# Optimization experiments

Hardware: AMD Instinct MI355X
Metric: run time of the kernel (lower is better)

The kernel has to match this reference:

```python
import jax, jax.numpy as jnp
import numpy as np

D_IN = 1024
D_OUT = 1024
H = 16            # head_cnt
G = 4             # attention_groups
LF = 2            # linformer_factor
HEAD_OUT = D_OUT // H          # 64 (value head dim)
DQ = HEAD_OUT // LF            # 32 (query/key head dim)
B, T = 2, 2048


def setup_inputs() -> dict:
    key = jax.random.key(0)
    ks = jax.random.split(key, 7)
    s = 0.02
    return {
        "x": jax.random.normal(ks[0], (B, T, D_IN), dtype=jnp.float32),
        "Wq": jax.random.normal(ks[1], (D_IN, D_OUT // LF), dtype=jnp.float32) * s,
        "Wk": jax.random.normal(ks[2], (D_IN, (D_OUT // LF) // G), dtype=jnp.float32) * s,
        "Wv": jax.random.normal(ks[3], (D_IN, D_OUT // G), dtype=jnp.float32) * s,
        "Wp": jax.random.normal(ks[4], (D_OUT, D_OUT), dtype=jnp.float32) * s,
        "bp": jnp.zeros((D_OUT,), dtype=jnp.float32),
    }


def _alibi_bias(T, dtype):
    # standard ALiBi slopes for H heads (H is a power of 2): m_h = 2^(-8h/H), h=1..H
    slopes = jnp.asarray(2.0 ** (-8.0 * np.arange(1, H + 1) / H), dtype=dtype)
    pos = jnp.arange(T)
    rel = (pos[None, :] - pos[:, None]).astype(dtype)  # j - i, <= 0 on causal part
    return slopes[:, None, None] * rel[None, :, :]      # (H, T, T)


def reference(x, Wq, Wk, Wv, Wp, bp):
    b, t, _ = x.shape
    q = x @ Wq                                  # (b, t, D_OUT/LF)
    k = jnp.tile(x @ Wk, (1, 1, G))             # repeat KV groups -> (b, t, D_OUT/LF)
    v = jnp.tile(x @ Wv, (1, 1, G))             # (b, t, D_OUT)

    q = q.reshape(b, t, H, DQ).transpose(0, 2, 1, 3)        # (b, H, t, DQ)
    k = k.reshape(b, t, H, DQ).transpose(0, 2, 1, 3)
    v = v.reshape(b, t, H, HEAD_OUT).transpose(0, 2, 1, 3)  # (b, H, t, HEAD_OUT)

    scores = jnp.einsum('bhqd,bhkd->bhqk', q, k)            # (b, H, t, t)
    causal = jnp.triu(jnp.ones((t, t), dtype=bool), k=1)
    scores = jnp.where(causal, -jnp.inf, scores)
    # faithful to source: alibi added after masking, then scaled by 1/sqrt(d_k)
    scores = (scores + _alibi_bias(t, scores.dtype)) / jnp.sqrt(jnp.asarray(DQ, scores.dtype))
    w = jax.nn.softmax(scores, axis=-1)
    ctx = jnp.einsum('bhqk,bhkd->bqhd', w, v).reshape(b, t, D_OUT)
    return ctx @ Wp + bp
```

## Files before the change

kernel.cpp:

```cpp
#include <hip/hip_runtime.h>
#include <hip/hip_bf16.h>

#define T_SEQ 2048
#define H_CNT 16
#define B_SZ  2
#define QKV_LD 896
#define KOFF   512
#define VOFF   640

typedef float  f32x4   __attribute__((ext_vector_type(4)));
typedef float  f32x16  __attribute__((ext_vector_type(16)));
typedef __bf16 bf16x8  __attribute__((ext_vector_type(8)));

static __device__ __forceinline__ ushort f2bf(float f) {
    union { float f; unsigned u; } v; v.f = f;
    unsigned u = v.u;
    unsigned r = (u + 0x7fffu + ((u >> 16) & 1u)) >> 16;
    return (ushort)r;
}
static __device__ __forceinline__ unsigned pack2bf(float a, float b) {
    union { __bf16 h[2]; unsigned u; } pk;
    pk.h[0] = (__bf16)a; pk.h[1] = (__bf16)b;
    return pk.u;
}

static __device__ __forceinline__ f32x4 mfma16(bf16x8 a, bf16x8 b, f32x4 c) {
    return __builtin_amdgcn_mfma_f32_16x16x32_bf16(a, b, c, 0, 0, 0);
}
static __device__ __forceinline__ f32x16 mfma32(bf16x8 a, bf16x8 b, f32x16 c) {
    return __builtin_amdgcn_mfma_f32_32x32x16_bf16(a, b, c, 0, 0, 0);
}

static __device__ __forceinline__ void gl_lds16(const void* g, void* l) {
    __builtin_amdgcn_global_load_lds((const __attribute__((address_space(1))) void*)g,
                                     (__attribute__((address_space(3))) void*)l, 16, 0, 0);
}

__global__ __launch_bounds__(256) void convert_bf16(const float* __restrict__ src,
                                                    ushort* __restrict__ dst) {
    const int i = blockIdx.x * 256 + threadIdx.x;
    const float4 v0 = reinterpret_cast<const float4*>(src)[i * 2];
    const float4 v1 = reinterpret_cast<const float4*>(src)[i * 2 + 1];
    uint4 o;
    o.x = (unsigned)f2bf(v0.x) | ((unsigned)f2bf(v0.y) << 16);
    o.y = (unsigned)f2bf(v0.z) | ((unsigned)f2bf(v0.w) << 16);
    o.z = (unsigned)f2bf(v1.x) | ((unsigned)f2bf(v1.y) << 16);
    o.w = (unsigned)f2bf(v1.z) | ((unsigned)f2bf(v1.w) << 16);
    reinterpret_cast<uint4*>(dst)[i] = o;
}

__global__ __launch_bounds__(256) void prep_weights(const float* __restrict__ Wq,
                                                    const float* __restrict__ Wk,
                                                    const float* __restrict__ Wv,
                                                    const float* __restrict__ Wp,
                                                    ushort* __restrict__ Wqkvt,
                                                    ushort* __restrict__ Wpt) {
    __shared__ float tile[32][33];
    const int x = blockIdx.x;
    const float* src; ushort* dst; int C, cx;
    if (x < 16)      { src = Wq; dst = Wqkvt;              C = 512;  cx = x; }
    else if (x < 20) { src = Wk; dst = Wqkvt + 512 * 1024; C = 128;  cx = x - 16; }
    else if (x < 28) { src = Wv; dst = Wqkvt + 640 * 1024; C = 256;  cx = x - 20; }
    else             { src = Wp; dst = Wpt;                C = 1024; cx = x - 28; }
    const int tx = threadIdx.x & 31, ty = threadIdx.x >> 5;
    const int r0 = blockIdx.y * 32, c0 = cx * 32;
#pragma unroll
    for (int i = 0; i < 32; i += 8)
        tile[ty + i][tx] = src[(size_t)(r0 + ty + i) * C + c0 + tx];
    __syncthreads();
#pragma unroll
    for (int i = 0; i < 32; i += 8)
        dst[(size_t)(c0 + ty + i) * 1024 + r0 + tx] = f2bf(tile[tx][ty + i]);
}

__global__ __launch_bounds__(256) void transpose_bf16_str(const ushort* __restrict__ src,
                                                          int src_ld, size_t src_zoff,
                                                          ushort* __restrict__ dst,
                                                          int R, int C, size_t dst_zoff) {
    __shared__ ushort tile[32][33];
    const int tx = threadIdx.x & 31, ty = threadIdx.x >> 5;
    const int r0 = blockIdx.y * 32, c0 = blockIdx.x * 32;
    const ushort* s = src + (size_t)blockIdx.z * src_zoff;
    ushort* d = dst + (size_t)blockIdx.z * dst_zoff;
#pragma unroll
    for (int i = 0; i < 32; i += 8)
        tile[ty + i][tx] = s[(size_t)(r0 + ty + i) * src_ld + c0 + tx];
    __syncthreads();
#pragma unroll
    for (int i = 0; i < 32; i += 8)
        d[(size_t)(c0 + ty + i) * R + r0 + tx] = tile[tx][ty + i];
}

template <bool OUT_BF16>
__global__ __launch_bounds__(256) void gemm_bf16(const ushort* __restrict__ A,
                                                 const ushort* __restrict__ Bt,
                                                 const float* __restrict__ bias,
                                                 void* __restrict__ Cout,
                                                 int M, int N, int K) {
    __shared__ __align__(16) ushort Aa[64 * 32], Ab[64 * 32];
    __shared__ __align__(16) ushort Ba[128 * 32], Bb[128 * 32];

    const int tid = threadIdx.x;
    const int w = tid >> 6, l = tid & 63;
    const int bm = blockIdx.y * 64, bn = blockIdx.x * 128;
    const int wr = (w >> 1) * 32, wc = (w & 1) * 64;
    const int lr = l & 15, lk = (l >> 4) * 8;
    const int crow = l >> 2, ck8 = (l & 3) * 8;

    const ushort* Ag  = A + (size_t)(bm + w * 16 + crow) * K + ck8;
    const ushort* Bg0 = Bt + (size_t)(bn + w * 16 + crow) * K + ck8;
    const ushort* Bg1 = Bt + (size_t)(bn + (w + 4) * 16 + crow) * K + ck8;
    ushort* Ala  = &Aa[w * 16 * 32];
    ushort* Alb  = &Ab[w * 16 * 32];
    ushort* Bl0a = &Ba[w * 16 * 32];
    ushort* Bl0b = &Bb[w * 16 * 32];
    ushort* Bl1a = &Ba[(w + 4) * 16 * 32];
    ushort* Bl1b = &Bb[(w + 4) * 16 * 32];

    f32x4 acc[2][4];
#pragma unroll
    for (int m = 0; m < 2; ++m)
#pragma unroll
        for (int n = 0; n < 4; ++n) acc[m][n] = (f32x4){0.f, 0.f, 0.f, 0.f};

    for (int k0 = 0; k0 < K; k0 += 64) {
        __syncthreads();
        gl_lds16(Ag + k0, Ala);
        gl_lds16(Ag + k0 + 32, Alb);
        gl_lds16(Bg0 + k0, Bl0a);
        gl_lds16(Bg0 + k0 + 32, Bl0b);
        gl_lds16(Bg1 + k0, Bl1a);
        gl_lds16(Bg1 + k0 + 32, Bl1b);
        __syncthreads();

        bf16x8 af0[2], af1[2], bf0[4], bf1[4];
#pragma unroll
        for (int m = 0; m < 2; ++m) {
            af0[m] = *reinterpret_cast<const bf16x8*>(&Aa[(wr + m * 16 + lr) * 32 + lk]);
            af1[m] = *reinterpret_cast<const bf16x8*>(&Ab[(wr + m * 16 + lr) * 32 + lk]);
        }
#pragma unroll
        for (int n = 0; n < 4; ++n) {
            bf0[n] = *reinterpret_cast<const bf16x8*>(&Ba[(wc + n * 16 + lr) * 32 + lk]);
            bf1[n] = *reinterpret_cast<const bf16x8*>(&Bb[(wc + n * 16 + lr) * 32 + lk]);
        }
#pragma unroll
        for (int m = 0; m < 2; ++m)
#pragma unroll
            for (int n = 0; n < 4; ++n) {
                acc[m][n] = mfma16(af0[m], bf0[n], acc[m][n]);
                acc[m][n] = mfma16(af1[m], bf1[n], acc[m][n]);
            }
    }

    const int orow = bm + wr + (l >> 4) * 4;
    const int ocol0 = bn + wc + lr;
#pragma unroll
    for (int m = 0; m < 2; ++m)
#pragma unroll
        for (int n = 0; n < 4; ++n) {
            const int col = ocol0 + n * 16;
            const float bv = OUT_BF16 ? 0.0f : bias[col];
#pragma unroll
            for (int r = 0; r < 4; ++r) {
                const size_t idx = (size_t)(orow + m * 16 + r) * N + col;
                if constexpr (OUT_BF16)
                    reinterpret_cast<ushort*>(Cout)[idx] = f2bf(acc[m][n][r]);
                else
                    reinterpret_cast<float*>(Cout)[idx] = acc[m][n][r] + bv;
            }
        }
}

#define LDK 40
#define LDV 136

__global__ __launch_bounds__(1024) void attn_mfma8(const ushort* __restrict__ qkv,
                                                   const ushort* __restrict__ vT,
                                                   ushort* __restrict__ ctx) {
    __shared__ __align__(16) ushort Ks[2][128 * LDK];
    __shared__ __align__(16) ushort Vs[2][64 * LDV];
    __shared__ float lsred[3][4][32];

    const int tid = threadIdx.x;
    const int w = tid >> 6, l = tid & 63;
    const int lq = l & 31;
    const int hi = l >> 5;
    const int tp = blockIdx.x, g = blockIdx.y, b = blockIdx.z;
    const int hd = w & 3, grp = w >> 2;
    const int h = g + 4 * hd;

    const float slope = exp2f(-0.5f * (float)(h + 1));
    const float k1 = 0.17677669529663687f * 1.4426950408889634f;
    const float k2 = slope * k1;
    const int Wint = (int)(275.0f / slope);

    const int ksd = tid >> 2, kc4 = tid & 3;
    const ushort* kgp = qkv + (size_t)b * T_SEQ * QKV_LD + KOFF + g * 32 +
                        (size_t)ksd * QKV_LD + kc4 * 8;
    const int sv = tid & 511;
    const int vsd = sv >> 3, vj = sv & 7;
    const int vs0 = (vj >> 2) << 1, vc4 = vj & 3;
    const int voff = (vc4 & 1) * 4 + (vc4 >> 1) * 16;
    const ushort* vgp = vT + ((size_t)b * 256 + g * 64 + vsd) * T_SEQ + vs0 * 32 + vc4 * 8;
    const int vl0 = vsd * LDV + vs0 * 32 + voff;
    const int vl1 = vsd * LDV + (vs0 + 1) * 32 + voff;

    float* slotA = reinterpret_cast<float*>(&Ks[0][0]);
    float* slotB = reinterpret_cast<float*>(&Vs[0][0]);
    float* slotC = reinterpret_cast<float*>(&Vs[1][0]);
    const int sidx = (hd * 64 + l) * 16;

    int cur = 0;
    for (int ph = 0; ph < 2; ++ph) {
        const int t = ph ? tp : (63 - tp);
        const int i0 = t * 32;
        const int nkeys = i0 + 32;
        const int jtmax = (nkeys + 127) & ~127;

        const ushort* qrow = qkv + ((size_t)(b * T_SEQ + i0 + lq)) * QKV_LD + h * 32 + hi * 8;
        const bf16x8 qa = *reinterpret_cast<const bf16x8*>(qrow);
        const bf16x8 qb = *reinterpret_cast<const bf16x8*>(qrow + 16);

        f32x16 o0, o1;
#pragma unroll
        for (int r = 0; r < 16; ++r) { o0[r] = 0.0f; o1[r] = 0.0f; }
        float ls = 0.0f;

        uint4 kreg, vr0, vr1;
        if (tid < 512) {
            kreg = *reinterpret_cast<const uint4*>(kgp);
        } else {
            vr0 = *reinterpret_cast<const uint4*>(vgp);
            vr1 = *reinterpret_cast<const uint4*>(vgp + 32);
        }

        for (int jt = 0; jt < jtmax; jt += 128) {
            if (tid < 512) {
                *reinterpret_cast<uint4*>(&Ks[cur][ksd * LDK + kc4 * 8]) = kreg;
            } else {
                *reinterpret_cast<uint2*>(&Vs[cur][vl0]) = make_uint2(vr0.x, vr0.y);
                *reinterpret_cast<uint2*>(&Vs[cur][vl0 + 8]) = make_uint2(vr0.z, vr0.w);
                *reinterpret_cast<uint2*>(&Vs[cur][vl1]) = make_uint2(vr1.x, vr1.y);
                *reinterpret_cast<uint2*>(&Vs[cur][vl1 + 8]) = make_uint2(vr1.z, vr1.w);
            }
            const int jn = jt + 128;
            if (jn < jtmax) {
                if (tid < 512) {
                    kreg = *reinterpret_cast<const uint4*>(kgp + (size_t)jn * QKV_LD);
                } else {
                    vr0 = *reinterpret_cast<const uint4*>(vgp + jn);
                    vr1 = *reinterpret_cast<const uint4*>(vgp + jn + 32);
                }
            }
            __syncthreads();

            const int jts = jt + 32 * grp;
            if (jts < nkeys && jts + 31 >= i0 - Wint) {
                const bf16x8 ka = *reinterpret_cast<const bf16x8*>(&Ks[cur][(grp * 32 + lq) * LDK + hi * 8]);
                const bf16x8 kb2 = *reinterpret_cast<const bf16x8*>(&Ks[cur][(grp * 32 + lq) * LDK + 16 + hi * 8]);
                f32x16 p;
#pragma unroll
                for (int r = 0; r < 16; ++r) p[r] = 0.0f;
                __builtin_amdgcn_s_setprio(1);
                p = mfma32(ka, qa, p);
                p = mfma32(kb2, qb, p);
                __builtin_amdgcn_s_setprio(0);

                const int dlt = jts + 4 * hi - i0 - lq;
                const float base2 = k2 * (float)dlt;
                float pe[16];
                if (jts + 31 > i0) {
#pragma unroll
                    for (int r = 0; r < 16; ++r) {
                        const int off = (r & 3) + 8 * (r >> 2);
                        const float arg = fmaf(p[r], k1, fmaf((float)off, k2, base2));
                        float e = exp2f(arg);
                        if (dlt + off > 0) e = 0.0f;
                        ls += e;
                        pe[r] = e;
                    }
                } else {
#pragma unroll
                    for (int r = 0; r < 16; ++r) {
                        const int off = (r & 3) + 8 * (r >> 2);
                        const float arg = fmaf(p[r], k1, fmaf((float)off, k2, base2));
                        const float e = exp2f(arg);
                        ls += e;
                        pe[r] = e;
                    }
                }
                union { unsigned u[4]; bf16x8 v; } A1, A2;
#pragma unroll
                for (int j2 = 0; j2 < 4; ++j2) A1.u[j2] = pack2bf(pe[2 * j2], pe[2 * j2 + 1]);
#pragma unroll
                for (int j2 = 0; j2 < 4; ++j2) A2.u[j2] = pack2bf(pe[8 + 2 * j2], pe[9 + 2 * j2]);

                const int vr0i = lq * LDV + grp * 32;
                const int vr1i = (32 + lq) * LDV + grp * 32;
                const bf16x8 v00 = *reinterpret_cast<const bf16x8*>(&Vs[cur][vr0i + hi * 8]);
                const bf16x8 v01 = *reinterpret_cast<const bf16x8*>(&Vs[cur][vr0i + 16 + hi * 8]);
                const bf16x8 v10 = *reinterpret_cast<const bf16x8*>(&Vs[cur][vr1i + hi * 8]);
                const bf16x8 v11 = *reinterpret_cast<const bf16x8*>(&Vs[cur][vr1i + 16 + hi * 8]);
                __builtin_amdgcn_s_setprio(1);
                o0 = mfma32(A1.v, v00, o0);
                o0 = mfma32(A2.v, v01, o0);
                o1 = mfma32(A1.v, v10, o1);
                o1 = mfma32(A2.v, v11, o1);
                __builtin_amdgcn_s_setprio(0);
            }
            cur ^= 1;
        }

        const float ls2 = ls + __shfl_xor(ls, 32);
        __syncthreads();
        if (grp) {
            float* sl = (grp == 1) ? slotA : (grp == 2) ? slotB : slotC;
#pragma unroll
            for (int r = 0; r < 16; ++r) sl[sidx + r] = o0[r];
            if (hi == 0) lsred[grp - 1][hd][lq] = ls2;
        }
        __syncthreads();
        float inv = 0.0f;
        if (grp == 0) {
#pragma unroll
            for (int r = 0; r < 16; ++r)
                o0[r] += slotA[sidx + r] + slotB[sidx + r] + slotC[sidx + r];
            inv = 1.0f / (ls2 + lsred[0][hd][lq] + lsred[1][hd][lq] + lsred[2][hd][lq]);
        }
        __syncthreads();
        if (grp) {
            float* sl = (grp == 1) ? slotA : (grp == 2) ? slotB : slotC;
#pragma unroll
            for (int r = 0; r < 16; ++r) sl[sidx + r] = o1[r];
        }
        __syncthreads();
        if (grp == 0) {
#pragma unroll
            for (int r = 0; r < 16; ++r)
                o1[r] += slotA[sidx + r] + slotB[sidx + r] + slotC[sidx + r];
#pragma unroll
            for (int r = 0; r < 16; ++r) {
                const int qr = (r & 3) + 8 * (r >> 2) + 4 * hi;
                const float invq = __shfl(inv, qr);
                const size_t row = (size_t)(b * T_SEQ + i0 + qr);
                ctx[row * 1024 + h * 64 + lq] = f2bf(o0[r] * invq);
                ctx[row * 1024 + h * 64 + 32 + lq] = f2bf(o1[r] * invq);
            }
        }
        __syncthreads();
    }
}

extern "C" void kernel_launch(void* const* d_in, const int* in_sizes, int n_in,
                              void* d_out, int out_size, void* d_ws, size_t ws_size,
                              hipStream_t stream) {
    const float* x  = (const float*)d_in[0];
    const float* Wq = (const float*)d_in[1];
    const float* Wk = (const float*)d_in[2];
    const float* Wv = (const float*)d_in[3];
    const float* Wp = (const float*)d_in[4];
    const float* bp = (const float*)d_in[5];

    const int M = B_SZ * T_SEQ;

    ushort* ws    = (ushort*)d_ws;
    ushort* xb    = ws;
    ushort* Wqkvt = xb + 4194304;
    ushort* Wpt   = Wqkvt + 917504;
    ushort* qkv   = Wpt + 1048576;
    ushort* vTb   = qkv + 3670016;
    ushort* cbuf  = vTb + 1048576;

    convert_bf16<<<2048, 256, 0, stream>>>(x, xb);
    prep_weights<<<dim3(60, 32), 256, 0, stream>>>(Wq, Wk, Wv, Wp, Wqkvt, Wpt);

    gemm_bf16<true><<<dim3(7, 64), 256, 0, stream>>>(xb, Wqkvt, nullptr, qkv, M, 896, 1024);

    transpose_bf16_str<<<dim3(8, 64, 2), 256, 0, stream>>>(
        qkv + VOFF, QKV_LD, (size_t)T_SEQ * QKV_LD, vTb, T_SEQ, 256, (size_t)256 * T_SEQ);

    attn_mfma8<<<dim3(32, 4, B_SZ), 1024, 0, stream>>>(qkv, vTb, cbuf);

    gemm_bf16<false><<<dim3(8, 64), 256, 0, stream>>>(cbuf, Wpt, bp, (float*)d_out, M, 1024, 1024);
}
```

Measured before the change: 100.9 us.

## Halve attention block to 512 threads, each wave handling two key sub-tiles

The attention kernel now runs with 512 threads instead of 1024, so each wave processes two 32-key sub-tiles per 128-key tile instead of one. Every thread loads both K and V, and loads past the causal key range are predicated off. The cross-wave reduction shrinks from four partial accumulators to two, cutting shared-memory traffic and barrier cost at the end. The trade-off is fewer waves per block to hide latency and more serial work per wave, on a grid of only 256 blocks.

```diff
diff --git a/kernel.cpp b/kernel.cpp
--- a/kernel.cpp
+++ b/kernel.cpp
@@ -175,12 +175,12 @@
 #define LDK 40
 #define LDV 136
 
-__global__ __launch_bounds__(1024) void attn_mfma8(const ushort* __restrict__ qkv,
-                                                   const ushort* __restrict__ vT,
-                                                   ushort* __restrict__ ctx) {
+__global__ __launch_bounds__(512) void attn_mfma9(const ushort* __restrict__ qkv,
+                                                  const ushort* __restrict__ vT,
+                                                  ushort* __restrict__ ctx) {
     __shared__ __align__(16) ushort Ks[2][128 * LDK];
     __shared__ __align__(16) ushort Vs[2][64 * LDV];
-    __shared__ float lsred[3][4][32];
+    __shared__ float lsred[4][32];
 
     const int tid = threadIdx.x;
     const int w = tid >> 6, l = tid & 63;
@@ -198,17 +198,14 @@
     const int ksd = tid >> 2, kc4 = tid & 3;
     const ushort* kgp = qkv + (size_t)b * T_SEQ * QKV_LD + KOFF + g * 32 +
                         (size_t)ksd * QKV_LD + kc4 * 8;
-    const int sv = tid & 511;
-    const int vsd = sv >> 3, vj = sv & 7;
+    const int vsd = tid >> 3, vj = tid & 7;
     const int vs0 = (vj >> 2) << 1, vc4 = vj & 3;
     const int voff = (vc4 & 1) * 4 + (vc4 >> 1) * 16;
     const ushort* vgp = vT + ((size_t)b * 256 + g * 64 + vsd) * T_SEQ + vs0 * 32 + vc4 * 8;
     const int vl0 = vsd * LDV + vs0 * 32 + voff;
     const int vl1 = vsd * LDV + (vs0 + 1) * 32 + voff;
 
-    float* slotA = reinterpret_cast<float*>(&Ks[0][0]);
-    float* slotB = reinterpret_cast<float*>(&Vs[0][0]);
-    float* slotC = reinterpret_cast<float*>(&Vs[1][0]);
+    float* red = reinterpret_cast<float*>(&Vs[0][0]);
     const int sidx = (hd * 64 + l) * 16;
 
     int cur = 0;
@@ -228,117 +225,111 @@
         float ls = 0.0f;
 
         uint4 kreg, vr0, vr1;
-        if (tid < 512) {
-            kreg = *reinterpret_cast<const uint4*>(kgp);
-        } else {
-            vr0 = *reinterpret_cast<const uint4*>(vgp);
-            vr1 = *reinterpret_cast<const uint4*>(vgp + 32);
-        }
+        if (ksd < nkeys) kreg = *reinterpret_cast<const uint4*>(kgp);
+        vr0 = *reinterpret_cast<const uint4*>(vgp);
+        if (vs0 * 32 + 32 < nkeys) vr1 = *reinterpret_cast<const uint4*>(vgp + 32);
 
         for (int jt = 0; jt < jtmax; jt += 128) {
-            if (tid < 512) {
-                *reinterpret_cast<uint4*>(&Ks[cur][ksd * LDK + kc4 * 8]) = kreg;
-            } else {
-                *reinterpret_cast<uint2*>(&Vs[cur][vl0]) = make_uint2(vr0.x, vr0.y);
-                *reinterpret_cast<uint2*>(&Vs[cur][vl0 + 8]) = make_uint2(vr0.z, vr0.w);
-                *reinterpret_cast<uint2*>(&Vs[cur][vl1]) = make_uint2(vr1.x, vr1.y);
-                *reinterpret_cast<uint2*>(&Vs[cur][vl1 + 8]) = make_uint2(vr1.z, vr1.w);
-            }
+            *reinterpret_cast<uint4*>(&Ks[cur][ksd * LDK + kc4 * 8]) = kreg;
+            *reinterpret_cast<uint2*>(&Vs[cur][vl0]) = make_uint2(vr0.x, vr0.y);
+            *reinterpret_cast<uint2*>(&Vs[cur][vl0 + 8]) = make_uint2(vr0.z, vr0.w);
+            *reinterpret_cast<uint2*>(&Vs[cur][vl1]) = make_uint2(vr1.x, vr1.y);
+            *reinterpret_cast<uint2*>(&Vs[cur][vl1 + 8]) = make_uint2(vr1.z, vr1.w);
             const int jn = jt + 128;
             if (jn < jtmax) {
-                if (tid < 512) {
+                if (jn + ksd < nkeys)
                     kreg = *reinterpret_cast<const uint4*>(kgp + (size_t)jn * QKV_LD);
-                } else {
+                if (jn + vs0 * 32 < nkeys)
                     vr0 = *reinterpret_cast<const uint4*>(vgp + jn);
+                if (jn + vs0 * 32 + 32 < nkeys)
                     vr1 = *reinterpret_cast<const uint4*>(vgp + jn + 32);
+            }
+            __syncthreads();
+
+#pragma unroll
+            for (int s = 0; s < 2; ++s) {
+                const int si = s * 2 + grp;
+                const int jts = jt + si * 32;
+                if (jts < nkeys && jts + 31 >= i0 - Wint) {
+                    const bf16x8 ka = *reinterpret_cast<const bf16x8*>(&Ks[cur][(si * 32 + lq) * LDK + hi * 8]);
+                    const bf16x8 kb2 = *reinterpret_cast<const bf16x8*>(&Ks[cur][(si * 32 + lq) * LDK + 16 + hi * 8]);
+                    f32x16 p;
+#pragma unroll
+                    for (int r = 0; r < 16; ++r) p[r] = 0.0f;
+                    __builtin_amdgcn_s_setprio(1);
+                    p = mfma32(ka, qa, p);
+                    p = mfma32(kb2, qb, p);
+                    __builtin_amdgcn_s_setprio(0);
+
+                    const int dlt = jts + 4 * hi - i0 - lq;
+                    const float base2 = k2 * (float)dlt;
+                    float pe[16];
+                    if (jts + 31 > i0) {
+#pragma unroll
+                        for (int r = 0; r < 16; ++r) {
+                            const int off = (r & 3) + 8 * (r >> 2);
+                            const float arg = fmaf(p[r], k1, fmaf((float)off, k2, base2));
+                            float e = exp2f(arg);
+                            if (dlt + off > 0) e = 0.0f;
+                            ls += e;
+                            pe[r] = e;
+                        }
+                    } else {
+#pragma unroll
+                        for (int r = 0; r < 16; ++r) {
+                            const int off = (r & 3) + 8 * (r >> 2);
+                            const float arg = fmaf(p[r], k1, fmaf((float)off, k2, base2));
+                            const float e = exp2f(arg);
+                            ls += e;
+                            pe[r] = e;
+                        }
+                    }
+                    union { unsigned u[4]; bf16x8 v; } A1, A2;
+#pragma unroll
+                    for (int j2 = 0; j2 < 4; ++j2) A1.u[j2] = pack2bf(pe[2 * j2], pe[2 * j2 + 1]);
+#pragma unroll
+                    for (int j2 = 0; j2 < 4; ++j2) A2.u[j2] = pack2bf(pe[8 + 2 * j2], pe[9 + 2 * j2]);
+
+                    const int vr0i = lq * LDV + si * 32;
+                    const int vr1i = (32 + lq) * LDV + si * 32;
+                    const bf16x8 v00 = *reinterpret_cast<const bf16x8*>(&Vs[cur][vr0i + hi * 8]);
+                    const bf16x8 v01 = *reinterpret_cast<const bf16x8*>(&Vs[cur][vr0i + 16 + hi * 8]);
+                    const bf16x8 v10 = *reinterpret_cast<const bf16x8*>(&Vs[cur][vr1i + hi * 8]);
+                    const bf16x8 v11 = *reinterpret_cast<const bf16x8*>(&Vs[cur][vr1i + 16 + hi * 8]);
+                    __builtin_amdgcn_s_setprio(1);
+                    o0 = mfma32(A1.v, v00, o0);
+                    o0 = mfma32(A2.v, v01, o0);
+                    o1 = mfma32(A1.v, v10, o1);
+                    o1 = mfma32(A2.v, v11, o1);
+                    __builtin_amdgcn_s_setprio(0);
                 }
             }
-            __syncthreads();
-
-            const int jts = jt + 32 * grp;
-            if (jts < nkeys && jts + 31 >= i0 - Wint) {
-                const bf16x8 ka = *reinterpret_cast<const bf16x8*>(&Ks[cur][(grp * 32 + lq) * LDK + hi * 8]);
-                const bf16x8 kb2 = *reinterpret_cast<const bf16x8*>(&Ks[cur][(grp * 32 + lq) * LDK + 16 + hi * 8]);
-                f32x16 p;
-#pragma unroll
-                for (int r = 0; r < 16; ++r) p[r] = 0.0f;
-                __builtin_amdgcn_s_setprio(1);
-                p = mfma32(ka, qa, p);
-                p = mfma32(kb2, qb, p);
-                __builtin_amdgcn_s_setprio(0);
-
-                const int dlt = jts + 4 * hi - i0 - lq;
-                const float base2 = k2 * (float)dlt;
-                float pe[16];
-                if (jts + 31 > i0) {
-#pragma unroll
-                    for (int r = 0; r < 16; ++r) {
-                        const int off = (r & 3) + 8 * (r >> 2);
-                        const float arg = fmaf(p[r], k1, fmaf((float)off, k2, base2));
-                        float e = exp2f(arg);
-                        if (dlt + off > 0) e = 0.0f;
-                        ls += e;
-                        pe[r] = e;
-                    }
-                } else {
-#pragma unroll
-                    for (int r = 0; r < 16; ++r) {
-                        const int off = (r & 3) + 8 * (r >> 2);
-                        const float arg = fmaf(p[r], k1, fmaf((float)off, k2, base2));
-                        const float e = exp2f(arg);
-                        ls += e;
-                        pe[r] = e;
-                    }
-                }
-                union { unsigned u[4]; bf16x8 v; } A1, A2;
-#pragma unroll
-                for (int j2 = 0; j2 < 4; ++j2) A1.u[j2] = pack2bf(pe[2 * j2], pe[2 * j2 + 1]);
-#pragma unroll
-                for (int j2 = 0; j2 < 4; ++j2) A2.u[j2] = pack2bf(pe[8 + 2 * j2], pe[9 + 2 * j2]);
-
-                const int vr0i = lq * LDV + grp * 32;
-                const int vr1i = (32 + lq) * LDV + grp * 32;
-                const bf16x8 v00 = *reinterpret_cast<const bf16x8*>(&Vs[cur][vr0i + hi * 8]);
-                const bf16x8 v01 = *reinterpret_cast<const bf16x8*>(&Vs[cur][vr0i + 16 + hi * 8]);
-                const bf16x8 v10 = *reinterpret_cast<const bf16x8*>(&Vs[cur][vr1i + hi * 8]);
-                const bf16x8 v11 = *reinterpret_cast<const bf16x8*>(&Vs[cur][vr1i + 16 + hi * 8]);
-                __builtin_amdgcn_s_setprio(1);
-                o0 = mfma32(A1.v, v00, o0);
-                o0 = mfma32(A2.v, v01, o0);
-                o1 = mfma32(A1.v, v10, o1);
-                o1 = mfma32(A2.v, v11, o1);
-                __builtin_amdgcn_s_setprio(0);
-            }
             cur ^= 1;
         }
 
         const float ls2 = ls + __shfl_xor(ls, 32);
         __syncthreads();
-        if (grp) {
-            float* sl = (grp == 1) ? slotA : (grp == 2) ? slotB : slotC;
-#pragma unroll
-            for (int r = 0; r < 16; ++r) sl[sidx + r] = o0[r];
-            if (hi == 0) lsred[grp - 1][hd][lq] = ls2;
+        if (grp == 0) {
+#pragma unroll
+            for (int r = 0; r < 16; ++r) red[sidx + r] = o0[r];
+            if (hi == 0) lsred[hd][lq] = ls2;
         }
         __syncthreads();
         float inv = 0.0f;
+        if (grp == 1) {
+#pragma unroll
+            for (int r = 0; r < 16; ++r) o0[r] += red[sidx + r];
+            inv = 1.0f / (ls2 + lsred[hd][lq]);
+        }
+        __syncthreads();
         if (grp == 0) {
 #pragma unroll
-            for (int r = 0; r < 16; ++r)
-                o0[r] += slotA[sidx + r] + slotB[sidx + r] + slotC[sidx + r];
-            inv = 1.0f / (ls2 + lsred[0][hd][lq] + lsred[1][hd][lq] + lsred[2][hd][lq]);
-        }
-        __syncthreads();
-        if (grp) {
-            float* sl = (grp == 1) ? slotA : (grp == 2) ? slotB : slotC;
-#pragma unroll
-            for (int r = 0; r < 16; ++r) sl[sidx + r] = o1[r];
-        }
-        __syncthreads();
-        if (grp == 0) {
-#pragma unroll
-            for (int r = 0; r < 16; ++r)
-                o1[r] += slotA[sidx + r] + slotB[sidx + r] + slotC[sidx + r];
+            for (int r = 0; r < 16; ++r) red[sidx + r] = o1[r];
+        }
+        __syncthreads();
+        if (grp == 1) {
+#pragma unroll
+            for (int r = 0; r < 16; ++r) o1[r] += red[sidx + r];
 #pragma unroll
             for (int r = 0; r < 16; ++r) {
                 const int qr = (r & 3) + 8 * (r >> 2) + 4 * hi;
@@ -380,7 +371,7 @@
     transpose_bf16_str<<<dim3(8, 64, 2), 256, 0, stream>>>(
         qkv + VOFF, QKV_LD, (size_t)T_SEQ * QKV_LD, vTb, T_SEQ, 256, (size_t)256 * T_SEQ);
 
-    attn_mfma8<<<dim3(32, 4, B_SZ), 1024, 0, stream>>>(qkv, vTb, cbuf);
+    attn_mfma9<<<dim3(32, 4, B_SZ), 512, 0, stream>>>(qkv, vTb, cbuf);
 
     gemm_bf16<false><<<dim3(8, 64), 256, 0, stream>>>(cbuf, Wpt, bp, (float*)d_out, M, 1024, 1024);
 }
```

After: 92.32 us. -8.5%, faster.
